# Kernel optimization log

Measured on AMD Instinct MI355X. Metric: run time of the kernel, lower is better.

Reference implementation:

```python
import jax, jax.numpy as jnp
import numpy as np

N = 100000   # nodes
D = 64       # in_features
E = 1200000  # edges (avg degree ~12)
C = 1.0      # curvature
MIN_NORM = 1e-15
PROJ_EPS = 4e-3  # float32 eps used by HGCN-style PoincareBall.proj


def setup_inputs() -> dict:
    key = jax.random.key(0)
    k1, k2, k3 = jax.random.split(key, 3)
    x = jax.random.normal(k1, (N, D), dtype=jnp.float32) * 0.1
    edge_index = jax.random.randint(k2, (2, E), 0, N, dtype=jnp.int32)
    # GCNConv learned params (lin weight + bias)
    W = jax.random.normal(k3, (D, D), dtype=jnp.float32) / np.sqrt(D)
    b = jnp.zeros((D,), dtype=jnp.float32)
    return {"x": x, "W": W, "b": b, "edge_index": edge_index}


def expmap0(u, c):
    sqrt_c = jnp.sqrt(c)
    u_norm = jnp.maximum(jnp.linalg.norm(u, axis=-1, keepdims=True), MIN_NORM)
    return jnp.tanh(sqrt_c * u_norm) * u / (sqrt_c * u_norm)


def proj(x, c):
    norm = jnp.maximum(jnp.linalg.norm(x, axis=-1, keepdims=True), MIN_NORM)
    maxnorm = (1.0 - PROJ_EPS) / jnp.sqrt(c)
    return jnp.where(norm > maxnorm, x / norm * maxnorm, x)


def gcn_conv(x, W, b, edge_index, n_nodes):
    # PyG GCNConv: h = x @ W; add self-loops; symmetric normalization; scatter-add; + bias
    h = x @ W  # [N, D]
    src, dst = edge_index[0], edge_index[1]
    loops = jnp.arange(n_nodes, dtype=edge_index.dtype)
    s = jnp.concatenate([src, loops])  # [E+N]
    d = jnp.concatenate([dst, loops])
    deg = jax.ops.segment_sum(jnp.ones(s.shape, dtype=h.dtype), d, num_segments=n_nodes)
    deg_inv_sqrt = jnp.where(deg > 0, deg ** -0.5, 0.0)
    norm = deg_inv_sqrt[s] * deg_inv_sqrt[d]  # [E+N]
    msgs = h[s] * norm[:, None]               # gather + scale: [E+N, D]
    out = jax.ops.segment_sum(msgs, d, num_segments=n_nodes)  # scatter-add
    return out + b


def reference(x, W, b, edge_index):
    # Note: original computes logmap0(x) but discards it (conv uses raw x) -- dead code.
    support_t = gcn_conv(x, W, b, edge_index, N)
    return proj(expmap0(support_t, C), C)
```

## Files before the change

### kernel.cpp

```cpp
#include <hip/hip_runtime.h>
#include <hip/hip_bf16.h>

#define DFEAT 64
#define NBSH  8
#define NPB   256
#define EPB   4096
#define CAPB  3584
#define REGS  4608

__global__ __launch_bounds__(256) void part_kernel(const int* __restrict__ ei,
                                                   int* __restrict__ bcnt,
                                                   unsigned* __restrict__ ebuf, int E) {
    __shared__ int h[512];
    __shared__ int base[512];
    int t = threadIdx.x;
    h[t] = 0; h[t + 256] = 0;
    __syncthreads();
    int bb = blockIdx.x * EPB;
    int sv[EPB / 256], dv[EPB / 256];
    #pragma unroll
    for (int i = 0; i < EPB / 256; ++i) {
        int e = bb + i * 256 + t;
        if (e < E) {
            sv[i] = ei[e];
            dv[i] = ei[E + e];
            atomicAdd(&h[dv[i] >> NBSH], 1);
        } else dv[i] = -1;
    }
    __syncthreads();
    base[t]       = h[t]       ? atomicAdd(&bcnt[t],       h[t])       : 0;
    base[t + 256] = h[t + 256] ? atomicAdd(&bcnt[t + 256], h[t + 256]) : 0;
    __syncthreads();
    h[t] = 0; h[t + 256] = 0;
    __syncthreads();
    #pragma unroll
    for (int i = 0; i < EPB / 256; ++i) {
        if (dv[i] >= 0) {
            int bkt = dv[i] >> NBSH;
            int pos = base[bkt] + atomicAdd(&h[bkt], 1);
            if (pos < CAPB)
                ebuf[(size_t)bkt * REGS + pos] =
                    (unsigned)sv[i] | ((unsigned)(dv[i] & (NPB - 1)) << 17);
        }
    }
}

__global__ __launch_bounds__(256) void csr_kernel(const int* __restrict__ bcnt,
                                                  unsigned* __restrict__ buf,
                                                  int* __restrict__ begs,
                                                  int* __restrict__ lens,
                                                  float* __restrict__ dinv,
                                                  const float* __restrict__ x,
                                                  unsigned* __restrict__ xs, int n) {
    __shared__ unsigned eb[CAPB];
    __shared__ int cnt[256];
    __shared__ int tmp[256];
    __shared__ float dish[256];
    int t = threadIdx.x, b = blockIdx.x;
    int ecnt = bcnt[b]; if (ecnt > CAPB) ecnt = CAPB;
    size_t rb = (size_t)b * REGS;
    for (int i = t; i < ecnt; i += 256) eb[i] = buf[rb + i];
    cnt[t] = 0;
    __syncthreads();
    for (int i = t; i < ecnt; i += 256) atomicAdd(&cnt[eb[i] >> 17], 1);
    __syncthreads();
    int nid = (b << NBSH) + t;
    int deg = cnt[t];
    int slots = (nid < n) ? ((deg + 4) & ~3) : 0;
    tmp[t] = slots;
    __syncthreads();
    int s = slots;
    for (int o = 1; o < 256; o <<= 1) {
        int y = (t >= o) ? tmp[t - o] : 0;
        __syncthreads();
        tmp[t] += y;
        __syncthreads();
    }
    int excl = tmp[t] - s;
    int beg = (int)rb + excl;
    float di = rsqrtf((float)(deg + 1));
    if (nid < n) {
        begs[nid] = beg;
        lens[nid] = slots;
        dinv[nid] = di;
        dish[t] = di;
        buf[beg] = (unsigned)nid;
        for (int k = deg + 1; k < slots; ++k) buf[beg + k] = (unsigned)n;
    }
    cnt[t] = excl + 1;
    __syncthreads();
    for (int i = t; i < ecnt; i += 256) {
        unsigned v = eb[i];
        int pos = atomicAdd(&cnt[v >> 17], 1);
        buf[rb + pos] = v & 0x1ffffu;
    }
    int rowlim = n - (b << NBSH);
    if (rowlim > 256) rowlim = 256;
    if (rowlim < 0) rowlim = 0;
    for (int i = t; i < (rowlim << 5); i += 256) {
        int rr = i >> 5, col = i & 31;
        int nid2 = (b << NBSH) + rr;
        float dd = dish[rr];
        float f0 = x[(size_t)nid2 * DFEAT + 2 * col] * dd;
        float f1 = x[(size_t)nid2 * DFEAT + 2 * col + 1] * dd;
        unsigned u0 = __float_as_uint(f0); u0 = (u0 + 0x7fffu + ((u0 >> 16) & 1u)) >> 16;
        unsigned u1 = __float_as_uint(f1); u1 = (u1 + 0x7fffu + ((u1 >> 16) & 1u)) >> 16;
        xs[(size_t)nid2 * 32 + col] = (u0 & 0xffffu) | (u1 << 16);
    }
    if (b == 0 && t < 32) xs[(size_t)n * 32 + t] = 0;
}

__global__ __launch_bounds__(256) void agg_kernel(const int* __restrict__ begs,
                                                  const int* __restrict__ lens,
                                                  const int* __restrict__ srcs,
                                                  const float* __restrict__ dinv,
                                                  const uint2* __restrict__ xs2,
                                                  const float* __restrict__ W,
                                                  const float* __restrict__ b,
                                                  float* __restrict__ out,
                                                  int n, int noctets) {
    __shared__ float Wl[DFEAT * DFEAT];
    __shared__ float xl[8][DFEAT];
    int t = threadIdx.x;
    #pragma unroll
    for (int i = 0; i < 16; ++i) Wl[i * 256 + t] = W[i * 256 + t];
    __syncthreads();

    int r = t >> 6, lane = t & 63;
    int g = lane >> 4;
    int q = lane & 15;
    float bias = b[lane];

    for (int oct = blockIdx.x; oct < noctets; oct += gridDim.x) {
        int na = oct * 8 + r;
        int nb_ = na + 4;
        bool va = na < n, vb = nb_ < n;
        if (!va) continue;

        int beg0 = begs[na],  end0 = beg0 + lens[na];
        int beg1 = 0, end1 = 0;
        if (vb) { beg1 = begs[nb_]; end1 = beg1 + lens[nb_]; }

        float a0 = 0, a1 = 0, a2 = 0, a3 = 0;
        float b0 = 0, b1 = 0, b2 = 0, b3 = 0;
        int base0 = beg0, base1 = beg1;
        while (base0 < end0 || base1 < end1) {
            int m0 = end0 - base0; m0 = m0 < 0 ? 0 : (m0 > 64 ? 64 : m0);
            int m1 = end1 - base1; m1 = m1 < 0 ? 0 : (m1 > 64 ? 64 : m1);
            int idx0 = 0, idx1 = 0;
            if (lane < m0) idx0 = srcs[base0 + lane];
            if (lane < m1) idx1 = srcs[base1 + lane];
            int q0 = m0 >> 2, q1 = m1 >> 2;
            int qc = q0 < q1 ? q0 : q1;
            #pragma unroll 4
            for (int j = 0; j < qc; ++j) {
                int sv0 = __shfl(idx0, 4 * j + g, 64);
                int sv1 = __shfl(idx1, 4 * j + g, 64);
                uint2 d0 = xs2[(unsigned)sv0 * 16 + q];
                uint2 d1 = xs2[(unsigned)sv1 * 16 + q];
                a0 += __uint_as_float(d0.x << 16);
                a1 += __uint_as_float(d0.x & 0xffff0000u);
                a2 += __uint_as_float(d0.y << 16);
                a3 += __uint_as_float(d0.y & 0xffff0000u);
                b0 += __uint_as_float(d1.x << 16);
                b1 += __uint_as_float(d1.x & 0xffff0000u);
                b2 += __uint_as_float(d1.y << 16);
                b3 += __uint_as_float(d1.y & 0xffff0000u);
            }
            #pragma unroll 4
            for (int j = qc; j < q0; ++j) {
                int sv0 = __shfl(idx0, 4 * j + g, 64);
                uint2 d0 = xs2[(unsigned)sv0 * 16 + q];
                a0 += __uint_as_float(d0.x << 16);
                a1 += __uint_as_float(d0.x & 0xffff0000u);
                a2 += __uint_as_float(d0.y << 16);
                a3 += __uint_as_float(d0.y & 0xffff0000u);
            }
            #pragma unroll 4
            for (int j = qc; j < q1; ++j) {
                int sv1 = __shfl(idx1, 4 * j + g, 64);
                uint2 d1 = xs2[(unsigned)sv1 * 16 + q];
                b0 += __uint_as_float(d1.x << 16);
                b1 += __uint_as_float(d1.x & 0xffff0000u);
                b2 += __uint_as_float(d1.y << 16);
                b3 += __uint_as_float(d1.y & 0xffff0000u);
            }
            base0 += 64; base1 += 64;
        }
        #pragma unroll
        for (int off = 16; off < 64; off <<= 1) {
            a0 += __shfl_xor(a0, off, 64);
            a1 += __shfl_xor(a1, off, 64);
            a2 += __shfl_xor(a2, off, 64);
            a3 += __shfl_xor(a3, off, 64);
            b0 += __shfl_xor(b0, off, 64);
            b1 += __shfl_xor(b1, off, 64);
            b2 += __shfl_xor(b2, off, 64);
            b3 += __shfl_xor(b3, off, 64);
        }
        if (g == 0) {
            float dia = dinv[na];
            xl[r][4 * q + 0] = a0 * dia;
            xl[r][4 * q + 1] = a1 * dia;
            xl[r][4 * q + 2] = a2 * dia;
            xl[r][4 * q + 3] = a3 * dia;
            if (vb) {
                float dib = dinv[nb_];
                xl[r + 4][4 * q + 0] = b0 * dib;
                xl[r + 4][4 * q + 1] = b1 * dib;
                xl[r + 4][4 * q + 2] = b2 * dib;
                xl[r + 4][4 * q + 3] = b3 * dib;
            }
        }

        float oa0 = bias, oa1 = 0.0f, ob0 = bias, ob1 = 0.0f;
        #pragma unroll
        for (int k = 0; k < DFEAT; k += 2) {
            float w0 = Wl[k * DFEAT + lane];
            float w1 = Wl[(k + 1) * DFEAT + lane];
            oa0 = fmaf(xl[r][k],     w0, oa0);
            oa1 = fmaf(xl[r][k + 1], w1, oa1);
            ob0 = fmaf(xl[r + 4][k],     w0, ob0);
            ob1 = fmaf(xl[r + 4][k + 1], w1, ob1);
        }
        float oa = oa0 + oa1;
        float ob = ob0 + ob1;

        float ssa = oa * oa, ssb = ob * ob;
        #pragma unroll
        for (int off = 32; off > 0; off >>= 1) {
            ssa += __shfl_xor(ssa, off, 64);
            ssb += __shfl_xor(ssb, off, 64);
        }
        float norma = fmaxf(sqrtf(ssa), 1e-15f);
        float sca = fminf(tanhf(norma), 1.0f - 4e-3f) / norma;
        out[(long long)na * DFEAT + lane] = oa * sca;
        if (vb) {
            float normb = fmaxf(sqrtf(ssb), 1e-15f);
            float scb = fminf(tanhf(normb), 1.0f - 4e-3f) / normb;
            out[(long long)nb_ * DFEAT + lane] = ob * scb;
        }
    }
}


extern "C" void kernel_launch(void* const* d_in, const int* in_sizes, int n_in,
                              void* d_out, int out_size, void* d_ws, size_t ws_size,
                              hipStream_t stream) {
    const float* x = (const float*)d_in[0];
    const float* W = (const float*)d_in[1];
    const float* b = (const float*)d_in[2];
    const int* ei  = (const int*)d_in[3];

    int n = in_sizes[0] / DFEAT;
    int E = in_sizes[3] / 2;
    int NBUCK = (n + NPB - 1) / NPB;
    int nblk = (E + EPB - 1) / EPB;
    int noctets = (n + 7) / 8;

    int* bcnt = (int*)d_ws;
    unsigned* buf = (unsigned*)(bcnt + 512);
    int* begs = (int*)(buf + (size_t)NBUCK * REGS);
    int* lens = begs + n;
    float* dinv = (float*)(lens + n);
    size_t xsoff = (size_t)(((int*)dinv + n) - (int*)d_ws);
    xsoff = (xsoff + 31) & ~(size_t)31;
    unsigned* xs = (unsigned*)d_ws + xsoff;

    float* out = (float*)d_out;

    int aggblocks = 2048;
    if (aggblocks > noctets) aggblocks = noctets;

    hipMemsetAsync(bcnt, 0, 512 * sizeof(int), stream);
    part_kernel<<<nblk, 256, 0, stream>>>(ei, bcnt, buf, E);
    csr_kernel <<<NBUCK, 256, 0, stream>>>(bcnt, buf, begs, lens, dinv, x, xs, n);
    agg_kernel <<<aggblocks, 256, 0, stream>>>(begs, lens, (const int*)buf, dinv,
                                               (const uint2*)xs, W, b, out, n, noctets);
}
```

Measured before the change: 184.2 us.

## Compute degrees with global atomics and split x-scaling into separate parallel blocks

The partition kernel now also counts per-node in-degree with global atomics, so the CSR stage no longer needs a shared-memory histogram pass over each bucket. The bf16 pre-scaling of x moves out of the per-bucket CSR blocks into extra independent blocks of the same launch, spreading that work over many more blocks instead of 391 bucket blocks. Edges per partition block are halved for more parallelism, and bucket loads use uint4 vector reads. The cost is 1.2M extra global atomics and a larger memset of the degree array.

Measured after the change: 220.9 us. 1.2x slower.

```diff
diff --git a/kernel.cpp b/kernel.cpp
--- a/kernel.cpp
+++ b/kernel.cpp
@@ -4,11 +4,13 @@
 #define DFEAT 64
 #define NBSH  8
 #define NPB   256
-#define EPB   4096
+#define EPB   2048
+#define EPT   (EPB / 256)
 #define CAPB  3584
 #define REGS  4608
 
 __global__ __launch_bounds__(256) void part_kernel(const int* __restrict__ ei,
+                                                   int* __restrict__ deg,
                                                    int* __restrict__ bcnt,
                                                    unsigned* __restrict__ ebuf, int E) {
     __shared__ int h[512];
@@ -17,14 +19,15 @@
     h[t] = 0; h[t + 256] = 0;
     __syncthreads();
     int bb = blockIdx.x * EPB;
-    int sv[EPB / 256], dv[EPB / 256];
+    int sv[EPT], dv[EPT];
     #pragma unroll
-    for (int i = 0; i < EPB / 256; ++i) {
+    for (int i = 0; i < EPT; ++i) {
         int e = bb + i * 256 + t;
         if (e < E) {
             sv[i] = ei[e];
             dv[i] = ei[E + e];
             atomicAdd(&h[dv[i] >> NBSH], 1);
+            atomicAdd(&deg[dv[i]], 1);
         } else dv[i] = -1;
     }
     __syncthreads();
@@ -34,7 +37,7 @@
     h[t] = 0; h[t + 256] = 0;
     __syncthreads();
     #pragma unroll
-    for (int i = 0; i < EPB / 256; ++i) {
+    for (int i = 0; i < EPT; ++i) {
         if (dv[i] >= 0) {
             int bkt = dv[i] >> NBSH;
             int pos = base[bkt] + atomicAdd(&h[bkt], 1);
@@ -45,28 +48,51 @@
     }
 }
 
-__global__ __launch_bounds__(256) void csr_kernel(const int* __restrict__ bcnt,
-                                                  unsigned* __restrict__ buf,
-                                                  int* __restrict__ begs,
-                                                  int* __restrict__ lens,
-                                                  float* __restrict__ dinv,
-                                                  const float* __restrict__ x,
-                                                  unsigned* __restrict__ xs, int n) {
+__global__ __launch_bounds__(256) void prep_kernel(const int* __restrict__ deg,
+                                                   const int* __restrict__ bcnt,
+                                                   unsigned* __restrict__ buf,
+                                                   int* __restrict__ begs,
+                                                   int* __restrict__ lens,
+                                                   float* __restrict__ dinv,
+                                                   const float* __restrict__ x,
+                                                   unsigned* __restrict__ xs,
+                                                   int n, int nbuck) {
     __shared__ unsigned eb[CAPB];
+    __shared__ int tmp[256];
     __shared__ int cnt[256];
-    __shared__ int tmp[256];
-    __shared__ float dish[256];
-    int t = threadIdx.x, b = blockIdx.x;
+    int t = threadIdx.x;
+
+    if ((int)blockIdx.x >= nbuck) {
+        int i = ((int)blockIdx.x - nbuck) * 256 + t;
+        int total = (n + 1) * 32;
+        if (i >= total) return;
+        int row = i >> 5, col = i & 31;
+        unsigned v = 0;
+        if (row < n) {
+            float di = rsqrtf((float)(deg[row] + 1));
+            if (col == 0) dinv[row] = di;
+            float f0 = x[(size_t)row * DFEAT + 2 * col] * di;
+            float f1 = x[(size_t)row * DFEAT + 2 * col + 1] * di;
+            unsigned u0 = __float_as_uint(f0); u0 = (u0 + 0x7fffu + ((u0 >> 16) & 1u)) >> 16;
+            unsigned u1 = __float_as_uint(f1); u1 = (u1 + 0x7fffu + ((u1 >> 16) & 1u)) >> 16;
+            v = (u0 & 0xffffu) | (u1 << 16);
+        }
+        xs[i] = v;
+        return;
+    }
+
+    int b = blockIdx.x;
+    size_t rb = (size_t)b * REGS;
     int ecnt = bcnt[b]; if (ecnt > CAPB) ecnt = CAPB;
-    size_t rb = (size_t)b * REGS;
-    for (int i = t; i < ecnt; i += 256) eb[i] = buf[rb + i];
-    cnt[t] = 0;
-    __syncthreads();
-    for (int i = t; i < ecnt; i += 256) atomicAdd(&cnt[eb[i] >> 17], 1);
-    __syncthreads();
+
+    const uint4* bufv = (const uint4*)(buf + rb);
+    uint4* ebv = (uint4*)eb;
+    int nv = (ecnt + 3) >> 2;
+    for (int i = t; i < nv; i += 256) ebv[i] = bufv[i];
+
     int nid = (b << NBSH) + t;
-    int deg = cnt[t];
-    int slots = (nid < n) ? ((deg + 4) & ~3) : 0;
+    int d = (nid < n) ? deg[nid] : 0;
+    int slots = (nid < n) ? ((d + 4) & ~3) : 0;
     tmp[t] = slots;
     __syncthreads();
     int s = slots;
@@ -78,14 +104,11 @@
     }
     int excl = tmp[t] - s;
     int beg = (int)rb + excl;
-    float di = rsqrtf((float)(deg + 1));
     if (nid < n) {
         begs[nid] = beg;
         lens[nid] = slots;
-        dinv[nid] = di;
-        dish[t] = di;
         buf[beg] = (unsigned)nid;
-        for (int k = deg + 1; k < slots; ++k) buf[beg + k] = (unsigned)n;
+        for (int k = d + 1; k < slots; ++k) buf[beg + k] = (unsigned)n;
     }
     cnt[t] = excl + 1;
     __syncthreads();
@@ -94,20 +117,6 @@
         int pos = atomicAdd(&cnt[v >> 17], 1);
         buf[rb + pos] = v & 0x1ffffu;
     }
-    int rowlim = n - (b << NBSH);
-    if (rowlim > 256) rowlim = 256;
-    if (rowlim < 0) rowlim = 0;
-    for (int i = t; i < (rowlim << 5); i += 256) {
-        int rr = i >> 5, col = i & 31;
-        int nid2 = (b << NBSH) + rr;
-        float dd = dish[rr];
-        float f0 = x[(size_t)nid2 * DFEAT + 2 * col] * dd;
-        float f1 = x[(size_t)nid2 * DFEAT + 2 * col + 1] * dd;
-        unsigned u0 = __float_as_uint(f0); u0 = (u0 + 0x7fffu + ((u0 >> 16) & 1u)) >> 16;
-        unsigned u1 = __float_as_uint(f1); u1 = (u1 + 0x7fffu + ((u1 >> 16) & 1u)) >> 16;
-        xs[(size_t)nid2 * 32 + col] = (u0 & 0xffffu) | (u1 << 16);
-    }
-    if (b == 0 && t < 32) xs[(size_t)n * 32 + t] = 0;
 }
 
 __global__ __launch_bounds__(256) void agg_kernel(const int* __restrict__ begs,
@@ -257,8 +266,10 @@
     int NBUCK = (n + NPB - 1) / NPB;
     int nblk = (E + EPB - 1) / EPB;
     int noctets = (n + 7) / 8;
-
-    int* bcnt = (int*)d_ws;
+    int np = (n + 3) & ~3;
+
+    int* deg  = (int*)d_ws;
+    int* bcnt = deg + np;
     unsigned* buf = (unsigned*)(bcnt + 512);
     int* begs = (int*)(buf + (size_t)NBUCK * REGS);
     int* lens = begs + n;
@@ -271,10 +282,12 @@
 
     int aggblocks = 2048;
     if (aggblocks > noctets) aggblocks = noctets;
-
-    hipMemsetAsync(bcnt, 0, 512 * sizeof(int), stream);
-    part_kernel<<<nblk, 256, 0, stream>>>(ei, bcnt, buf, E);
-    csr_kernel <<<NBUCK, 256, 0, stream>>>(bcnt, buf, begs, lens, dinv, x, xs, n);
+    int xsblocks = ((n + 1) * 32 + 255) / 256;
+
+    hipMemsetAsync(deg, 0, (size_t)(np + 512) * sizeof(int), stream);
+    part_kernel<<<nblk, 256, 0, stream>>>(ei, deg, bcnt, buf, E);
+    prep_kernel<<<NBUCK + xsblocks, 256, 0, stream>>>(deg, bcnt, buf, begs, lens,
+                                                      dinv, x, xs, n, NBUCK);
     agg_kernel <<<aggblocks, 256, 0, stream>>>(begs, lens, (const int*)buf, dinv,
                                                (const uint2*)xs, W, b, out, n, noctets);
 }
```
